# Kernel tuning notes

Measured on AMD Instinct MI355X. Metric: run time of the kernel, lower is better.

The kernel has to match this reference:

```python
import jax, jax.numpy as jnp
import numpy as np

N = 50000      # num nodes
E = 800000     # num edges
D = 64         # in_dim = hid_dim = out_dim
K = 8          # propagation hops (num_layers)
ALPHA = 0.6


def setup_inputs() -> dict:
    key = jax.random.key(0)
    ks = jax.random.split(key, 6)
    s = 1.0 / np.sqrt(D)
    return {
        "x": jax.random.normal(ks[0], (N, D), jnp.float32),
        "w_conv": jax.random.normal(ks[1], (D, D), jnp.float32) * s,
        "b_conv": jnp.zeros((D,), jnp.float32),
        "w1": jax.random.normal(ks[2], (D, D), jnp.float32) * s,
        "b1": jnp.zeros((D,), jnp.float32),
        "w2": jax.random.normal(ks[3], (D, D), jnp.float32) * s,
        "b2": jnp.zeros((D,), jnp.float32),
        "edge_index": jax.random.randint(ks[4], (2, E), 0, N, jnp.int64),
    }


def _gcn_norm(edge_index, num_nodes):
    # add self loops, symmetric normalization D^-1/2 (A+I) D^-1/2
    loop = jnp.arange(num_nodes, dtype=edge_index.dtype)
    src = jnp.concatenate([edge_index[0], loop])
    dst = jnp.concatenate([edge_index[1], loop])
    ones = jnp.ones(src.shape[0], jnp.float32)
    deg = jax.ops.segment_sum(ones, dst, num_segments=num_nodes)
    dinv = jnp.where(deg > 0, jax.lax.rsqrt(deg), 0.0)
    norm = dinv[src] * dinv[dst]  # [E+N]
    return src, dst, norm


def reference(x, w_conv, b_conv, w1, b1, w2, b2, edge_index):
    num_nodes = x.shape[0]
    src, dst, norm = _gcn_norm(edge_index, num_nodes)
    # SSGConv: h = alpha*x + (1-alpha)/K * sum_k A_hat^k x
    h = ALPHA * x
    xk = x
    coef = (1.0 - ALPHA) / K
    for _ in range(K):
        xk = jax.ops.segment_sum(norm[:, None] * xk[src], dst, num_segments=num_nodes)
        h = h + coef * xk
    h = h @ w_conv.T + b_conv        # SSGConv's internal Linear
    h = jax.nn.relu(h)               # F.relu(conv1(...))
    h = jax.nn.relu(h @ w1.T + b1)   # lin1 + relu (dropout p=0, eval)
    return h @ w2.T + b2             # lin2
```

## Files before the change

kernel.cpp:

```cpp
#include <hip/hip_runtime.h>

#define DD 64
#define ALPHA 0.6f
#define KHOPS 8
#define WP 72

typedef __attribute__((ext_vector_type(8))) short bf16x8;
typedef __attribute__((ext_vector_type(4))) float f32x4;

static __device__ __forceinline__ unsigned short f2bf(float f) {
    unsigned int u = __float_as_uint(f);
    unsigned int r = (u + 0x7FFFu + ((u >> 16) & 1u)) >> 16;
    return (unsigned short)r;
}
static __device__ __forceinline__ unsigned int pack2bf(float lo, float hi) {
    return (unsigned int)f2bf(lo) | ((unsigned int)f2bf(hi) << 16);
}

__global__ __launch_bounds__(256) void zero_kernel(uint4* __restrict__ p, int n16) {
    int i = blockIdx.x * blockDim.x + threadIdx.x;
    if (i < n16) p[i] = make_uint4(0u, 0u, 0u, 0u);
}

#define FCHUNK 2048
__global__ __launch_bounds__(256) void deg_count_kernel(const int* __restrict__ dst,
                                                        int* __restrict__ cnt,
                                                        int e, int n) {
    int xcd = blockIdx.x & 7;
    int chunk = blockIdx.x >> 3;
    int lo = (int)(((long long)n * xcd) >> 3);
    int hi = (int)(((long long)n * (xcd + 1)) >> 3);
    int base = chunk * FCHUNK + threadIdx.x * 8;
    if (base >= e) return;
    int4 d0 = *(const int4*)(dst + base);
    int4 d1 = *(const int4*)(dst + base + 4);
    int dv[8] = {d0.x, d0.y, d0.z, d0.w, d1.x, d1.y, d1.z, d1.w};
    #pragma unroll
    for (int j = 0; j < 8; ++j) {
        if (base + j < e) {
            int d = dv[j];
            if (d >= lo && d < hi) atomicAdd(&cnt[d], 1);
        }
    }
}

__global__ __launch_bounds__(256) void scan1_kernel(const int* __restrict__ cnt,
                                                    int* __restrict__ partials,
                                                    float2* __restrict__ dinvr, int n) {
    int i = blockIdx.x * 256 + threadIdx.x;
    int v = (i < n) ? cnt[i] : 0;
    if (i < n) {
        float d = (float)(v + 1);
        dinvr[i] = make_float2(rsqrtf(d), sqrtf(d));
    }
    int sum = v;
    #pragma unroll
    for (int off = 1; off < 64; off <<= 1) sum += __shfl_down(sum, off, 64);
    __shared__ int ws[4];
    if ((threadIdx.x & 63) == 0) ws[threadIdx.x >> 6] = sum;
    __syncthreads();
    if (threadIdx.x == 0) partials[blockIdx.x] = ws[0] + ws[1] + ws[2] + ws[3];
}

__global__ __launch_bounds__(1024) void scan2_kernel(int* __restrict__ partials, int nb) {
    __shared__ int s[1024];
    int t = threadIdx.x;
    int v = (t < nb) ? partials[t] : 0;
    s[t] = v;
    __syncthreads();
    for (int off = 1; off < 1024; off <<= 1) {
        int tmp = (t >= off) ? s[t - off] : 0;
        __syncthreads();
        s[t] += tmp;
        __syncthreads();
    }
    if (t < nb) partials[t] = s[t] - v;
}

__global__ __launch_bounds__(256) void scan3_kernel(const int* __restrict__ cnt,
                                                    const int* __restrict__ partials,
                                                    int* __restrict__ rowptr,
                                                    int* __restrict__ cursor, int n) {
    int t = threadIdx.x;
    int i = blockIdx.x * 256 + t;
    int v = (i < n) ? cnt[i] : 0;
    int lane = t & 63;
    int incl = v;
    #pragma unroll
    for (int off = 1; off < 64; off <<= 1) {
        int u = __shfl_up(incl, off, 64);
        if (lane >= off) incl += u;
    }
    __shared__ int wsum[4];
    if (lane == 63) wsum[t >> 6] = incl;
    __syncthreads();
    int woff = 0;
    for (int w = 0; w < (t >> 6); ++w) woff += wsum[w];
    int excl = incl - v + woff + partials[blockIdx.x];
    if (i < n) { rowptr[i] = excl; cursor[i] = excl; }
    if (i == n - 1) rowptr[n] = excl + v;
}

__global__ __launch_bounds__(256) void fill_kernel(const int* __restrict__ src,
                                                   const int* __restrict__ dst,
                                                   int* __restrict__ cursor,
                                                   int* __restrict__ esrc, int e, int n) {
    int xcd = blockIdx.x & 7;
    int chunk = blockIdx.x >> 3;
    int lo = (int)(((long long)n * xcd) >> 3);
    int hi = (int)(((long long)n * (xcd + 1)) >> 3);
    int base = chunk * FCHUNK + threadIdx.x * 8;
    if (base >= e) return;
    int4 s0 = *(const int4*)(src + base);
    int4 s1 = *(const int4*)(src + base + 4);
    int4 d0 = *(const int4*)(dst + base);
    int4 d1 = *(const int4*)(dst + base + 4);
    int sv[8] = {s0.x, s0.y, s0.z, s0.w, s1.x, s1.y, s1.z, s1.w};
    int dv[8] = {d0.x, d0.y, d0.z, d0.w, d1.x, d1.y, d1.z, d1.w};
    #pragma unroll
    for (int j = 0; j < 8; ++j) {
        if (base + j < e) {
            int d = dv[j];
            if (d >= lo && d < hi) {
                int pos = atomicAdd(&cursor[d], 1);
                esrc[pos] = sv[j];
            }
        }
    }
}

__global__ __launch_bounds__(256) void init_kernel(const float4* __restrict__ x,
                                                   const float2* __restrict__ dinvr,
                                                   float4* __restrict__ h,
                                                   ushort4* __restrict__ yb, int n4) {
    int i = blockIdx.x * blockDim.x + threadIdx.x;
    if (i >= n4) return;
    int row = i >> 4;
    float di = dinvr[row].x;
    float4 v = x[i];
    h[i] = make_float4(ALPHA * v.x, ALPHA * v.y, ALPHA * v.z, ALPHA * v.w);
    ushort4 b;
    b.x = f2bf(di * v.x); b.y = f2bf(di * v.y);
    b.z = f2bf(di * v.z); b.w = f2bf(di * v.w);
    yb[i] = b;
}

static __device__ __forceinline__ void add8(float* acc, uint4 v) {
    acc[0] += __uint_as_float(v.x << 16);
    acc[1] += __uint_as_float(v.x & 0xffff0000u);
    acc[2] += __uint_as_float(v.y << 16);
    acc[3] += __uint_as_float(v.y & 0xffff0000u);
    acc[4] += __uint_as_float(v.z << 16);
    acc[5] += __uint_as_float(v.z & 0xffff0000u);
    acc[6] += __uint_as_float(v.w << 16);
    acc[7] += __uint_as_float(v.w & 0xffff0000u);
}

template <int DO_H, int DO_OUT>
__global__ __launch_bounds__(256) void hop_kernel(const int* __restrict__ rowptr,
                                                  const int* __restrict__ esrc,
                                                  const float2* __restrict__ dinvr,
                                                  const unsigned short* __restrict__ yin,
                                                  unsigned short* __restrict__ yout,
                                                  float* __restrict__ h,
                                                  float coef, int n) {
    int wid = (blockIdx.x * blockDim.x + threadIdx.x) >> 6;
    if (wid >= n) return;
    int lane = threadIdx.x & 63;
    int g = lane >> 3;
    int s = lane & 7;
    int node = wid;

    int e0 = rowptr[node];
    int e1 = rowptr[node + 1];

    float acc[8] = {0.f, 0.f, 0.f, 0.f, 0.f, 0.f, 0.f, 0.f};
    float yprev[8];
    float2 dr;

    if (g == 0) {
        dr = dinvr[node];
        uint4 v = *(const uint4*)(yin + (size_t)node * 64 + s * 8);
        yprev[0] = __uint_as_float(v.x << 16);
        yprev[1] = __uint_as_float(v.x & 0xffff0000u);
        yprev[2] = __uint_as_float(v.y << 16);
        yprev[3] = __uint_as_float(v.y & 0xffff0000u);
        yprev[4] = __uint_as_float(v.z << 16);
        yprev[5] = __uint_as_float(v.z & 0xffff0000u);
        yprev[6] = __uint_as_float(v.w << 16);
        yprev[7] = __uint_as_float(v.w & 0xffff0000u);
        #pragma unroll
        for (int j = 0; j < 8; ++j) acc[j] = yprev[j];
    }

    int deg = e1 - e0;
    int niter = (deg + 7) >> 3;
    int clampe = e1 - 1;
    for (int i = 0; i < niter; i += 4) {
        int eA = e0 + (i << 3) + g;
        int eB = eA + 8, eC = eA + 16, eD = eA + 24;
        bool vA = eA < e1, vB = eB < e1, vC = eC < e1, vD = eD < e1;
        int sA = esrc[vA ? eA : clampe];
        int sB = esrc[vB ? eB : clampe];
        int sC = esrc[vC ? eC : clampe];
        int sD = esrc[vD ? eD : clampe];
        uint4 va = *(const uint4*)(yin + (size_t)sA * 64 + s * 8);
        uint4 vb = *(const uint4*)(yin + (size_t)sB * 64 + s * 8);
        uint4 vc = *(const uint4*)(yin + (size_t)sC * 64 + s * 8);
        uint4 vd = *(const uint4*)(yin + (size_t)sD * 64 + s * 8);
        if (!vA) va = make_uint4(0u, 0u, 0u, 0u);
        if (!vB) vb = make_uint4(0u, 0u, 0u, 0u);
        if (!vC) vc = make_uint4(0u, 0u, 0u, 0u);
        if (!vD) vd = make_uint4(0u, 0u, 0u, 0u);
        add8(acc, va);
        add8(acc, vb);
        add8(acc, vc);
        add8(acc, vd);
    }

    #pragma unroll
    for (int off = 8; off < 64; off <<= 1) {
        #pragma unroll
        for (int j = 0; j < 8; ++j) acc[j] += __shfl_xor(acc[j], off, 64);
    }

    if (g == 0) {
        float di = dr.x;
        float d2 = di * di;
        if (DO_OUT) {
            uint4 o;
            o.x = pack2bf(d2 * acc[0], d2 * acc[1]);
            o.y = pack2bf(d2 * acc[2], d2 * acc[3]);
            o.z = pack2bf(d2 * acc[4], d2 * acc[5]);
            o.w = pack2bf(d2 * acc[6], d2 * acc[7]);
            *(uint4*)(yout + (size_t)node * 64 + s * 8) = o;
        }
        if (DO_H) {
            float rd = dr.y;
            float* hp = h + (size_t)node * 64 + s * 8;
            float4 h0 = *(float4*)hp;
            float4 h1 = *(float4*)(hp + 4);
            h0.x += coef * (rd * yprev[0] + di * acc[0]);
            h0.y += coef * (rd * yprev[1] + di * acc[1]);
            h0.z += coef * (rd * yprev[2] + di * acc[2]);
            h0.w += coef * (rd * yprev[3] + di * acc[3]);
            h1.x += coef * (rd * yprev[4] + di * acc[4]);
            h1.y += coef * (rd * yprev[5] + di * acc[5]);
            h1.z += coef * (rd * yprev[6] + di * acc[6]);
            h1.w += coef * (rd * yprev[7] + di * acc[7]);
            *(float4*)hp = h0;
            *(float4*)(hp + 4) = h1;
        }
    }
}

__global__ __launch_bounds__(256) void mlp_mfma_kernel(const float* __restrict__ hin,
                                                       const float* __restrict__ wc,
                                                       const float* __restrict__ bc,
                                                       const float* __restrict__ w1,
                                                       const float* __restrict__ b1,
                                                       const float* __restrict__ w2,
                                                       const float* __restrict__ b2,
                                                       float* __restrict__ out, int n) {
    __shared__ unsigned short wlds[3][64][WP];
    __shared__ unsigned short xlds[64][WP];
    int t = threadIdx.x;

    const float* wm[3] = {wc, w1, w2};
    #pragma unroll
    for (int m = 0; m < 3; ++m) {
        const float4* w4 = (const float4*)wm[m];
        #pragma unroll
        for (int k = 0; k < 4; ++k) {
            int fid = t + k * 256;
            int j = fid >> 4, c4 = fid & 15;
            float4 v = w4[fid];
            *(uint2*)&wlds[m][j][c4 * 4] =
                make_uint2(pack2bf(v.x, v.y), pack2bf(v.z, v.w));
        }
    }

    int r0 = blockIdx.x * 64;
    const float4* h4 = (const float4*)hin;
    #pragma unroll
    for (int k = 0; k < 4; ++k) {
        int fid = t + k * 256;
        int r = fid >> 4, c4 = fid & 15;
        int gr = r0 + r;
        float4 v = (gr < n) ? h4[(size_t)gr * 16 + c4]
                            : make_float4(0.f, 0.f, 0.f, 0.f);
        *(uint2*)&xlds[r][c4 * 4] = make_uint2(pack2bf(v.x, v.y), pack2bf(v.z, v.w));
    }
    __syncthreads();

    int lane = t & 63;
    int wv = t >> 6;
    int rbase = wv * 16;
    int lr = lane & 15;
    int kg = lane >> 4;
    const float* bias[3] = {bc, b1, b2};

    #pragma unroll
    for (int m = 0; m < 3; ++m) {
        bf16x8 a0 = *(bf16x8*)&xlds[rbase + lr][kg * 8];
        bf16x8 a1 = *(bf16x8*)&xlds[rbase + lr][32 + kg * 8];
        #pragma unroll
        for (int ct = 0; ct < 4; ++ct) {
            bf16x8 bv0 = *(bf16x8*)&wlds[m][ct * 16 + lr][kg * 8];
            bf16x8 bv1 = *(bf16x8*)&wlds[m][ct * 16 + lr][32 + kg * 8];
            f32x4 acc = {0.f, 0.f, 0.f, 0.f};
            acc = __builtin_amdgcn_mfma_f32_16x16x32_bf16(a0, bv0, acc, 0, 0, 0);
            acc = __builtin_amdgcn_mfma_f32_16x16x32_bf16(a1, bv1, acc, 0, 0, 0);
            float bb = bias[m][ct * 16 + lr];
            if (m < 2) {
                #pragma unroll
                for (int rg = 0; rg < 4; ++rg) {
                    float v = fmaxf(acc[rg] + bb, 0.0f);
                    xlds[rbase + kg * 4 + rg][ct * 16 + lr] = f2bf(v);
                }
            } else {
                #pragma unroll
                for (int rg = 0; rg < 4; ++rg) {
                    int gr = r0 + rbase + kg * 4 + rg;
                    if (gr < n) out[(size_t)gr * 64 + ct * 16 + lr] = acc[rg] + bb;
                }
            }
        }
    }
}

extern "C" void kernel_launch(void* const* d_in, const int* in_sizes, int n_in,
                              void* d_out, int out_size, void* d_ws, size_t ws_size,
                              hipStream_t stream) {
    const float* x      = (const float*)d_in[0];
    const float* w_conv = (const float*)d_in[1];
    const float* b_conv = (const float*)d_in[2];
    const float* w1     = (const float*)d_in[3];
    const float* b1     = (const float*)d_in[4];
    const float* w2     = (const float*)d_in[5];
    const float* b2     = (const float*)d_in[6];
    const int*   ei     = (const int*)d_in[7];

    int n = in_sizes[0] / DD;
    int e = in_sizes[7] / 2;
    const int* src = ei;
    const int* dst = ei + e;

    char* wsb = (char*)d_ws;
    int*    cnt      = (int*)(wsb + 0);
    float2* dinvr    = (float2*)(wsb + 256 * 1024);
    int*    rowptr   = (int*)(wsb + 768 * 1024);
    int*    cursor   = (int*)(wsb + 1024 * 1024);
    int*    partials = (int*)(wsb + 1280 * 1024);
    int*    esrc     = (int*)(wsb + 1344 * 1024);
    unsigned short* yb0 = (unsigned short*)(wsb + 1344 * 1024 + (size_t)e * 4);
    unsigned short* yb1 = yb0 + (size_t)n * DD;
    float* h = (float*)d_out;

    const int B = 256;
    int n4 = n * (DD / 4);
    int nb = (n + 255) / 256;
    int nchunks = (e + FCHUNK - 1) / FCHUNK;

    int n16 = (n + 3) / 4;
    zero_kernel<<<(n16 + B - 1) / B, B, 0, stream>>>((uint4*)cnt, n16);
    deg_count_kernel<<<nchunks * 8, B, 0, stream>>>(dst, cnt, e, n);
    scan1_kernel<<<nb, B, 0, stream>>>(cnt, partials, dinvr, n);
    scan2_kernel<<<1, 1024, 0, stream>>>(partials, nb);
    scan3_kernel<<<nb, B, 0, stream>>>(cnt, partials, rowptr, cursor, n);
    fill_kernel<<<nchunks * 8, B, 0, stream>>>(src, dst, cursor, esrc, e, n);

    init_kernel<<<(n4 + B - 1) / B, B, 0, stream>>>(
        (const float4*)x, dinvr, (float4*)h, (ushort4*)yb0, n4);

    float coef = (1.0f - ALPHA) / (float)KHOPS;
    int hblocks = (int)(((size_t)n * 64 + B - 1) / B);

    unsigned short* cur = yb0;
    unsigned short* nxt = yb1;
    for (int k = 1; k <= KHOPS; ++k) {
        if (k == KHOPS)
            hop_kernel<1, 0><<<hblocks, B, 0, stream>>>(rowptr, esrc, dinvr, cur, nxt,
                                                        h, coef, n);
        else if (k % 2 == 0)
            hop_kernel<1, 1><<<hblocks, B, 0, stream>>>(rowptr, esrc, dinvr, cur, nxt,
                                                        h, coef, n);
        else
            hop_kernel<0, 1><<<hblocks, B, 0, stream>>>(rowptr, esrc, dinvr, cur, nxt,
                                                        h, coef, n);
        unsigned short* tmp = cur; cur = nxt; nxt = tmp;
    }

    mlp_mfma_kernel<<<(n + 63) / 64, B, 0, stream>>>(h, w_conv, b_conv, w1, b1,
                                                     w2, b2, (float*)d_out, n);
}
```

Measured before the change: 277.7 us.

## Split bf16 features into column halves and map XCDs to slice-partitioned node ranges

Stores the bf16 propagated features as two separate 32-column slabs instead of interleaved 64-column rows. Each hop block is assigned, by its blockIdx modulo 8 (presumably the XCD), one slab and a quarter of the node range. The intent is for each XCD's L2 to cache only half the feature matrix so gather reuse is higher. The cost is that every node's edge list is walked twice (once per slab), which doubles the index loads and per-node overhead. Each wave now processes 16 edges per step with 4 lanes per row.

```diff
diff --git a/kernel.cpp b/kernel.cpp
--- a/kernel.cpp
+++ b/kernel.cpp
@@ -132,17 +132,18 @@
 __global__ __launch_bounds__(256) void init_kernel(const float4* __restrict__ x,
                                                    const float2* __restrict__ dinvr,
                                                    float4* __restrict__ h,
-                                                   ushort4* __restrict__ yb, int n4) {
+                                                   unsigned short* __restrict__ yb,
+                                                   int n4, int n) {
     int i = blockIdx.x * blockDim.x + threadIdx.x;
     if (i >= n4) return;
     int row = i >> 4;
+    int c4 = i & 15;
     float di = dinvr[row].x;
     float4 v = x[i];
     h[i] = make_float4(ALPHA * v.x, ALPHA * v.y, ALPHA * v.z, ALPHA * v.w);
-    ushort4 b;
-    b.x = f2bf(di * v.x); b.y = f2bf(di * v.y);
-    b.z = f2bf(di * v.z); b.w = f2bf(di * v.w);
-    yb[i] = b;
+    int sl = c4 >> 3;
+    unsigned short* dstp = yb + (size_t)sl * n * 32 + (size_t)row * 32 + (c4 & 7) * 4;
+    *(uint2*)dstp = make_uint2(pack2bf(di * v.x, di * v.y), pack2bf(di * v.z, di * v.w));
 }
 
 static __device__ __forceinline__ void add8(float* acc, uint4 v) {
@@ -164,12 +165,18 @@
                                                   unsigned short* __restrict__ yout,
                                                   float* __restrict__ h,
                                                   float coef, int n) {
-    int wid = (blockIdx.x * blockDim.x + threadIdx.x) >> 6;
-    if (wid >= n) return;
+    int xcd = blockIdx.x & 7;
+    int sl = xcd & 1;
+    int q = xcd >> 1;
+    int qlo = (int)(((long long)n * q) >> 2);
+    int qhi = (int)(((long long)n * (q + 1)) >> 2);
+    int node = qlo + ((blockIdx.x >> 3) << 2) + (threadIdx.x >> 6);
+    if (node >= qhi) return;
     int lane = threadIdx.x & 63;
-    int g = lane >> 3;
-    int s = lane & 7;
-    int node = wid;
+    int g = lane >> 2;
+    int s = lane & 3;
+
+    const unsigned short* ybase = yin + (size_t)sl * n * 32;
 
     int e0 = rowptr[node];
     int e1 = rowptr[node + 1];
@@ -180,7 +187,7 @@
 
     if (g == 0) {
         dr = dinvr[node];
-        uint4 v = *(const uint4*)(yin + (size_t)node * 64 + s * 8);
+        uint4 v = *(const uint4*)(ybase + (size_t)node * 32 + s * 8);
         yprev[0] = __uint_as_float(v.x << 16);
         yprev[1] = __uint_as_float(v.x & 0xffff0000u);
         yprev[2] = __uint_as_float(v.y << 16);
@@ -194,32 +201,24 @@
     }
 
     int deg = e1 - e0;
-    int niter = (deg + 7) >> 3;
+    int niter = (deg + 15) >> 4;
     int clampe = e1 - 1;
-    for (int i = 0; i < niter; i += 4) {
-        int eA = e0 + (i << 3) + g;
-        int eB = eA + 8, eC = eA + 16, eD = eA + 24;
-        bool vA = eA < e1, vB = eB < e1, vC = eC < e1, vD = eD < e1;
+    for (int i = 0; i < niter; i += 2) {
+        int eA = e0 + (i << 4) + g;
+        int eB = eA + 16;
+        bool vA = eA < e1, vB = eB < e1;
         int sA = esrc[vA ? eA : clampe];
         int sB = esrc[vB ? eB : clampe];
-        int sC = esrc[vC ? eC : clampe];
-        int sD = esrc[vD ? eD : clampe];
-        uint4 va = *(const uint4*)(yin + (size_t)sA * 64 + s * 8);
-        uint4 vb = *(const uint4*)(yin + (size_t)sB * 64 + s * 8);
-        uint4 vc = *(const uint4*)(yin + (size_t)sC * 64 + s * 8);
-        uint4 vd = *(const uint4*)(yin + (size_t)sD * 64 + s * 8);
+        uint4 va = *(const uint4*)(ybase + (size_t)sA * 32 + s * 8);
+        uint4 vb = *(const uint4*)(ybase + (size_t)sB * 32 + s * 8);
         if (!vA) va = make_uint4(0u, 0u, 0u, 0u);
         if (!vB) vb = make_uint4(0u, 0u, 0u, 0u);
-        if (!vC) vc = make_uint4(0u, 0u, 0u, 0u);
-        if (!vD) vd = make_uint4(0u, 0u, 0u, 0u);
         add8(acc, va);
         add8(acc, vb);
-        add8(acc, vc);
-        add8(acc, vd);
-    }
-
-    #pragma unroll
-    for (int off = 8; off < 64; off <<= 1) {
+    }
+
+    #pragma unroll
+    for (int off = 4; off < 64; off <<= 1) {
         #pragma unroll
         for (int j = 0; j < 8; ++j) acc[j] += __shfl_xor(acc[j], off, 64);
     }
@@ -233,11 +232,11 @@
             o.y = pack2bf(d2 * acc[2], d2 * acc[3]);
             o.z = pack2bf(d2 * acc[4], d2 * acc[5]);
             o.w = pack2bf(d2 * acc[6], d2 * acc[7]);
-            *(uint4*)(yout + (size_t)node * 64 + s * 8) = o;
+            *(uint4*)(yout + (size_t)sl * n * 32 + (size_t)node * 32 + s * 8) = o;
         }
         if (DO_H) {
             float rd = dr.y;
-            float* hp = h + (size_t)node * 64 + s * 8;
+            float* hp = h + (size_t)node * 64 + sl * 32 + s * 8;
             float4 h0 = *(float4*)hp;
             float4 h1 = *(float4*)(hp + 4);
             h0.x += coef * (rd * yprev[0] + di * acc[0]);
@@ -371,23 +370,25 @@
     fill_kernel<<<nchunks * 8, B, 0, stream>>>(src, dst, cursor, esrc, e, n);
 
     init_kernel<<<(n4 + B - 1) / B, B, 0, stream>>>(
-        (const float4*)x, dinvr, (float4*)h, (ushort4*)yb0, n4);
+        (const float4*)x, dinvr, (float4*)h, yb0, n4, n);
 
     float coef = (1.0f - ALPHA) / (float)KHOPS;
-    int hblocks = (int)(((size_t)n * 64 + B - 1) / B);
+    int qmax = (n + 3) >> 2;
+    int bpx = (qmax + 3) >> 2;
+    int hgrid = bpx * 8;
 
     unsigned short* cur = yb0;
     unsigned short* nxt = yb1;
     for (int k = 1; k <= KHOPS; ++k) {
         if (k == KHOPS)
-            hop_kernel<1, 0><<<hblocks, B, 0, stream>>>(rowptr, esrc, dinvr, cur, nxt,
-                                                        h, coef, n);
+            hop_kernel<1, 0><<<hgrid, B, 0, stream>>>(rowptr, esrc, dinvr, cur, nxt,
+                                                      h, coef, n);
         else if (k % 2 == 0)
-            hop_kernel<1, 1><<<hblocks, B, 0, stream>>>(rowptr, esrc, dinvr, cur, nxt,
-                                                        h, coef, n);
+            hop_kernel<1, 1><<<hgrid, B, 0, stream>>>(rowptr, esrc, dinvr, cur, nxt,
+                                                      h, coef, n);
         else
-            hop_kernel<0, 1><<<hblocks, B, 0, stream>>>(rowptr, esrc, dinvr, cur, nxt,
-                                                        h, coef, n);
+            hop_kernel<0, 1><<<hgrid, B, 0, stream>>>(rowptr, esrc, dinvr, cur, nxt,
+                                                      h, coef, n);
         unsigned short* tmp = cur; cur = nxt; nxt = tmp;
     }
 
```

Result: slower. 396.1 us (+42.6%).

## Store all hop outputs and fold h accumulation into MLP prologue

Applied to the files above, without the earlier changes.

Each hop now writes its scaled bf16 output to its own buffer. The MLP kernel rebuilds h as alpha*x plus coef times the sum of all eight hop buffers. This removes the fp32 h read-modify-write from the hop kernels and the h write from init. In exchange the workspace needs K+1 bf16 copies, the MLP kernel reads eight bf16 rows per node, and h is now accumulated from bf16-rounded hop outputs.

```diff
diff --git a/kernel.cpp b/kernel.cpp
--- a/kernel.cpp
+++ b/kernel.cpp
@@ -131,14 +131,12 @@
 
 __global__ __launch_bounds__(256) void init_kernel(const float4* __restrict__ x,
                                                    const float2* __restrict__ dinvr,
-                                                   float4* __restrict__ h,
                                                    ushort4* __restrict__ yb, int n4) {
     int i = blockIdx.x * blockDim.x + threadIdx.x;
     if (i >= n4) return;
     int row = i >> 4;
     float di = dinvr[row].x;
     float4 v = x[i];
-    h[i] = make_float4(ALPHA * v.x, ALPHA * v.y, ALPHA * v.z, ALPHA * v.w);
     ushort4 b;
     b.x = f2bf(di * v.x); b.y = f2bf(di * v.y);
     b.z = f2bf(di * v.z); b.w = f2bf(di * v.w);
@@ -156,14 +154,12 @@
     acc[7] += __uint_as_float(v.w & 0xffff0000u);
 }
 
-template <int DO_H, int DO_OUT>
 __global__ __launch_bounds__(256) void hop_kernel(const int* __restrict__ rowptr,
                                                   const int* __restrict__ esrc,
                                                   const float2* __restrict__ dinvr,
                                                   const unsigned short* __restrict__ yin,
                                                   unsigned short* __restrict__ yout,
-                                                  float* __restrict__ h,
-                                                  float coef, int n) {
+                                                  int n) {
     int wid = (blockIdx.x * blockDim.x + threadIdx.x) >> 6;
     if (wid >= n) return;
     int lane = threadIdx.x & 63;
@@ -175,22 +171,13 @@
     int e1 = rowptr[node + 1];
 
     float acc[8] = {0.f, 0.f, 0.f, 0.f, 0.f, 0.f, 0.f, 0.f};
-    float yprev[8];
-    float2 dr;
+    float d2 = 0.f;
 
     if (g == 0) {
-        dr = dinvr[node];
+        float di = dinvr[node].x;
+        d2 = di * di;
         uint4 v = *(const uint4*)(yin + (size_t)node * 64 + s * 8);
-        yprev[0] = __uint_as_float(v.x << 16);
-        yprev[1] = __uint_as_float(v.x & 0xffff0000u);
-        yprev[2] = __uint_as_float(v.y << 16);
-        yprev[3] = __uint_as_float(v.y & 0xffff0000u);
-        yprev[4] = __uint_as_float(v.z << 16);
-        yprev[5] = __uint_as_float(v.z & 0xffff0000u);
-        yprev[6] = __uint_as_float(v.w << 16);
-        yprev[7] = __uint_as_float(v.w & 0xffff0000u);
-        #pragma unroll
-        for (int j = 0; j < 8; ++j) acc[j] = yprev[j];
+        add8(acc, v);
     }
 
     int deg = e1 - e0;
@@ -225,36 +212,19 @@
     }
 
     if (g == 0) {
-        float di = dr.x;
-        float d2 = di * di;
-        if (DO_OUT) {
-            uint4 o;
-            o.x = pack2bf(d2 * acc[0], d2 * acc[1]);
-            o.y = pack2bf(d2 * acc[2], d2 * acc[3]);
-            o.z = pack2bf(d2 * acc[4], d2 * acc[5]);
-            o.w = pack2bf(d2 * acc[6], d2 * acc[7]);
-            *(uint4*)(yout + (size_t)node * 64 + s * 8) = o;
-        }
-        if (DO_H) {
-            float rd = dr.y;
-            float* hp = h + (size_t)node * 64 + s * 8;
-            float4 h0 = *(float4*)hp;
-            float4 h1 = *(float4*)(hp + 4);
-            h0.x += coef * (rd * yprev[0] + di * acc[0]);
-            h0.y += coef * (rd * yprev[1] + di * acc[1]);
-            h0.z += coef * (rd * yprev[2] + di * acc[2]);
-            h0.w += coef * (rd * yprev[3] + di * acc[3]);
-            h1.x += coef * (rd * yprev[4] + di * acc[4]);
-            h1.y += coef * (rd * yprev[5] + di * acc[5]);
-            h1.z += coef * (rd * yprev[6] + di * acc[6]);
-            h1.w += coef * (rd * yprev[7] + di * acc[7]);
-            *(float4*)hp = h0;
-            *(float4*)(hp + 4) = h1;
-        }
-    }
-}
-
-__global__ __launch_bounds__(256) void mlp_mfma_kernel(const float* __restrict__ hin,
+        uint4 o;
+        o.x = pack2bf(d2 * acc[0], d2 * acc[1]);
+        o.y = pack2bf(d2 * acc[2], d2 * acc[3]);
+        o.z = pack2bf(d2 * acc[4], d2 * acc[5]);
+        o.w = pack2bf(d2 * acc[6], d2 * acc[7]);
+        *(uint4*)(yout + (size_t)node * 64 + s * 8) = o;
+    }
+}
+
+__global__ __launch_bounds__(256) void mlp_mfma_kernel(const float* __restrict__ x,
+                                                       const float2* __restrict__ dinvr,
+                                                       const unsigned short* __restrict__ yall,
+                                                       size_t ystride, float coef,
                                                        const float* __restrict__ wc,
                                                        const float* __restrict__ bc,
                                                        const float* __restrict__ w1,
@@ -281,15 +251,32 @@
     }
 
     int r0 = blockIdx.x * 64;
-    const float4* h4 = (const float4*)hin;
+    const float4* x4 = (const float4*)x;
     #pragma unroll
     for (int k = 0; k < 4; ++k) {
         int fid = t + k * 256;
         int r = fid >> 4, c4 = fid & 15;
         int gr = r0 + r;
-        float4 v = (gr < n) ? h4[(size_t)gr * 16 + c4]
-                            : make_float4(0.f, 0.f, 0.f, 0.f);
-        *(uint2*)&xlds[r][c4 * 4] = make_uint2(pack2bf(v.x, v.y), pack2bf(v.z, v.w));
+        float h0 = 0.f, h1 = 0.f, h2 = 0.f, h3 = 0.f;
+        if (gr < n) {
+            float4 xv = x4[(size_t)gr * 16 + c4];
+            float ys0 = 0.f, ys1 = 0.f, ys2 = 0.f, ys3 = 0.f;
+            #pragma unroll
+            for (int kk = 1; kk <= KHOPS; ++kk) {
+                uint2 u = *(const uint2*)(yall + (size_t)kk * ystride +
+                                          (size_t)gr * 64 + c4 * 4);
+                ys0 += __uint_as_float(u.x << 16);
+                ys1 += __uint_as_float(u.x & 0xffff0000u);
+                ys2 += __uint_as_float(u.y << 16);
+                ys3 += __uint_as_float(u.y & 0xffff0000u);
+            }
+            float cr = coef * dinvr[gr].y;
+            h0 = ALPHA * xv.x + cr * ys0;
+            h1 = ALPHA * xv.y + cr * ys1;
+            h2 = ALPHA * xv.z + cr * ys2;
+            h3 = ALPHA * xv.w + cr * ys3;
+        }
+        *(uint2*)&xlds[r][c4 * 4] = make_uint2(pack2bf(h0, h1), pack2bf(h2, h3));
     }
     __syncthreads();
 
@@ -353,9 +340,8 @@
     int*    cursor   = (int*)(wsb + 1024 * 1024);
     int*    partials = (int*)(wsb + 1280 * 1024);
     int*    esrc     = (int*)(wsb + 1344 * 1024);
-    unsigned short* yb0 = (unsigned short*)(wsb + 1344 * 1024 + (size_t)e * 4);
-    unsigned short* yb1 = yb0 + (size_t)n * DD;
-    float* h = (float*)d_out;
+    unsigned short* ybase = (unsigned short*)(wsb + 1344 * 1024 + (size_t)e * 4);
+    size_t ystride = (size_t)n * DD;
 
     const int B = 256;
     int n4 = n * (DD / 4);
@@ -371,26 +357,18 @@
     fill_kernel<<<nchunks * 8, B, 0, stream>>>(src, dst, cursor, esrc, e, n);
 
     init_kernel<<<(n4 + B - 1) / B, B, 0, stream>>>(
-        (const float4*)x, dinvr, (float4*)h, (ushort4*)yb0, n4);
+        (const float4*)x, dinvr, (ushort4*)ybase, n4);
 
     float coef = (1.0f - ALPHA) / (float)KHOPS;
     int hblocks = (int)(((size_t)n * 64 + B - 1) / B);
 
-    unsigned short* cur = yb0;
-    unsigned short* nxt = yb1;
     for (int k = 1; k <= KHOPS; ++k) {
-        if (k == KHOPS)
-            hop_kernel<1, 0><<<hblocks, B, 0, stream>>>(rowptr, esrc, dinvr, cur, nxt,
-                                                        h, coef, n);
-        else if (k % 2 == 0)
-            hop_kernel<1, 1><<<hblocks, B, 0, stream>>>(rowptr, esrc, dinvr, cur, nxt,
-                                                        h, coef, n);
-        else
-            hop_kernel<0, 1><<<hblocks, B, 0, stream>>>(rowptr, esrc, dinvr, cur, nxt,
-                                                        h, coef, n);
-        unsigned short* tmp = cur; cur = nxt; nxt = tmp;
-    }
-
-    mlp_mfma_kernel<<<(n + 63) / 64, B, 0, stream>>>(h, w_conv, b_conv, w1, b1,
-                                                     w2, b2, (float*)d_out, n);
-}
+        hop_kernel<<<hblocks, B, 0, stream>>>(rowptr, esrc, dinvr,
+                                              ybase + (size_t)(k - 1) * ystride,
+                                              ybase + (size_t)k * ystride, n);
+    }
+
+    mlp_mfma_kernel<<<(n + 63) / 64, B, 0, stream>>>(
+        x, dinvr, ybase, ystride, coef, w_conv, b_conv, w1, b1, w2, b2,
+        (float*)d_out, n);
+}
```

After: 274.8 us. Within noise of the previous version (-1.1%).
